# Kernel tuning notes

Hardware: AMD Instinct MI355X
Metric: run time of the kernel (lower is better)

Reference implementation:

```python
import jax, jax.numpy as jnp
import numpy as np

B, DIM, HID = 16384, 1024, 2048


def _ln(x, g, b, eps=1e-5):
    m = x.mean(-1, keepdims=True)
    v = ((x - m) ** 2).mean(-1, keepdims=True)
    return (x - m) / jnp.sqrt(v + eps) * g + b


def _attn1(x_kv, Wv, bv, Wo, bo):
    # seq-len-1 MHA: softmax over a single key is exactly 1 (per head),
    # so output = out_proj(v_proj(kv)); q/k projections cancel identically.
    return (x_kv @ Wv.T + bv) @ Wo.T + bo


def _ffn(x, W1, b1, W2, b2):
    return jnp.maximum(x @ W1.T + b1, 0.0) @ W2.T + b2


def setup_inputs() -> dict:
    key = jax.random.key(0)
    ks = iter(jax.random.split(key, 32))
    s = 0.02
    d = {
        'visual_feat': jax.random.normal(next(ks), (B, DIM), jnp.float32),
        'text_feat': jax.random.normal(next(ks), (B, DIM), jnp.float32),
    }
    for tag in ('sv', 'st', 'v2t', 't2v'):
        d[f'Wv_{tag}'] = jax.random.normal(next(ks), (DIM, DIM), jnp.float32) * s
        d[f'bv_{tag}'] = jnp.zeros((DIM,), jnp.float32)
        d[f'Wo_{tag}'] = jax.random.normal(next(ks), (DIM, DIM), jnp.float32) * s
        d[f'bo_{tag}'] = jnp.zeros((DIM,), jnp.float32)
    for tag in ('v1', 't1', 'v2', 't2'):
        d[f'g_{tag}'] = jnp.ones((DIM,), jnp.float32)
        d[f'be_{tag}'] = jnp.zeros((DIM,), jnp.float32)
    for tag in ('v', 't'):
        d[f'W1_{tag}'] = jax.random.normal(next(ks), (HID, DIM), jnp.float32) * s
        d[f'b1_{tag}'] = jnp.zeros((HID,), jnp.float32)
        d[f'W2_{tag}'] = jax.random.normal(next(ks), (DIM, HID), jnp.float32) * s
        d[f'b2_{tag}'] = jnp.zeros((DIM,), jnp.float32)
    return d


def reference(visual_feat, text_feat,
              Wv_sv, bv_sv, Wo_sv, bo_sv,
              Wv_st, bv_st, Wo_st, bo_st,
              Wv_v2t, bv_v2t, Wo_v2t, bo_v2t,
              Wv_t2v, bv_t2v, Wo_t2v, bo_t2v,
              g_v1, be_v1, g_t1, be_t1, g_v2, be_v2, g_t2, be_t2,
              W1_v, b1_v, W2_v, b2_v, W1_t, b1_t, W2_t, b2_t):
    v_self = _ln(visual_feat + _attn1(visual_feat, Wv_sv, bv_sv, Wo_sv, bo_sv), g_v1, be_v1)
    t_self = _ln(text_feat + _attn1(text_feat, Wv_st, bv_st, Wo_st, bo_st), g_t1, be_t1)
    v_cross = _attn1(t_self, Wv_v2t, bv_v2t, Wo_v2t, bo_v2t)  # v queries t -> depends on kv=t_self only
    t_cross = _attn1(v_self, Wv_t2v, bv_t2v, Wo_t2v, bo_t2v)
    v_fused = _ln(visual_feat + (v_self + v_cross) * 0.5, g_v2, be_v2)
    t_fused = _ln(text_feat + (t_self + t_cross) * 0.5, g_t2, be_t2)
    v_out = v_fused + _ffn(v_fused, W1_v, b1_v, W2_v, b2_v)
    t_out = t_fused + _ffn(t_fused, W1_t, b1_t, W2_t, b2_t)
    new_context = (v_out + t_out) * 0.5
    return (v_out, t_out, new_context)
```

## Files before the change

kernel.cpp:

```cpp
#include <hip/hip_runtime.h>
#include <stdint.h>


typedef unsigned short u16;
typedef __bf16 bf16x8 __attribute__((ext_vector_type(8)));
typedef float f32x4 __attribute__((ext_vector_type(4)));

__device__ __forceinline__ u16 f2bf(float f) {
    uint32_t x = __float_as_uint(f);
    uint32_t r = (x + 0x7fffu + ((x >> 16) & 1u)) >> 16;
    return (u16)r;
}
__device__ __forceinline__ float bf2f(u16 u) {
    return __uint_as_float(((uint32_t)u) << 16);
}

__device__ __forceinline__ void glds16(const u16* g, u16* l) {
    __builtin_amdgcn_global_load_lds(
        (__attribute__((address_space(1))) void*)g,
        (__attribute__((address_space(3))) void*)l, 16, 0, 0);
}

__global__ __launch_bounds__(256) void cvtk(const float* __restrict__ src,
                                            u16* __restrict__ dst) {
    size_t i = ((size_t)blockIdx.x * 256 + threadIdx.x) * 4;
    float4 v = *(const float4*)&src[i];
    ushort4 o;
    o.x = f2bf(v.x); o.y = f2bf(v.y); o.z = f2bf(v.z); o.w = f2bf(v.w);
    *(ushort4*)&dst[i] = o;
}

struct Ptr4 { const float* p[4]; };
__global__ __launch_bounds__(256) void tcvtk(Ptr4 src, u16* __restrict__ dst) {
    __shared__ float t[32][33];
    const int z = blockIdx.z;
    const float* s = src.p[z];
    const int bx = blockIdx.x * 32, by = blockIdx.y * 32;
    const int tx = threadIdx.x & 31, ty = threadIdx.x >> 5;
#pragma unroll
    for (int i = 0; i < 32; i += 8)
        t[ty + i][tx] = s[(size_t)(by + ty + i) * 1024 + bx + tx];
    __syncthreads();
    u16* d = dst + (size_t)z * (1024 * 1024);
#pragma unroll
    for (int i = 0; i < 32; i += 8)
        d[(size_t)(bx + ty + i) * 1024 + by + tx] = f2bf(t[tx][ty + i]);
}

struct BiasArgs { const float* Wo[4]; const float* bv[4]; const float* bo[4]; };
__global__ __launch_bounds__(256) void biask(BiasArgs a, float* __restrict__ out) {
    const int z = blockIdx.y;
    const int row = blockIdx.x * 4 + (threadIdx.x >> 6);
    const int lane = threadIdx.x & 63;
    const float* w = a.Wo[z] + (size_t)row * 1024 + lane * 16;
    const float* v = a.bv[z] + lane * 16;
    float s = 0.f;
#pragma unroll
    for (int i = 0; i < 16; i += 4) {
        float4 w4 = *(const float4*)&w[i];
        float4 v4 = *(const float4*)&v[i];
        s += w4.x * v4.x + w4.y * v4.y + w4.z * v4.z + w4.w * v4.w;
    }
#pragma unroll
    for (int o = 1; o < 64; o <<= 1) s += __shfl_xor(s, o);
    if (lane == 0) out[(size_t)z * 1024 + row] = s + a.bo[z][row];
}

__global__ __launch_bounds__(256) void ctxk(const float* __restrict__ a,
                                            const float* __restrict__ b,
                                            float* __restrict__ o) {
    size_t i = ((size_t)blockIdx.x * 256 + threadIdx.x) * 4;
    float4 va = *(const float4*)&a[i];
    float4 vb = *(const float4*)&b[i];
    float4 vo;
    vo.x = 0.5f * (va.x + vb.x); vo.y = 0.5f * (va.y + vb.y);
    vo.z = 0.5f * (va.z + vb.z); vo.w = 0.5f * (va.w + vb.w);
    *(float4*)&o[i] = vo;
}

__global__ __launch_bounds__(256) void ln_kernel(
    const float* __restrict__ x, const u16* __restrict__ a1,
    const u16* __restrict__ a2, float s,
    const float* __restrict__ g, const float* __restrict__ be,
    u16* __restrict__ out) {
    const int tid = threadIdx.x;
    const size_t base = (size_t)blockIdx.x * 1024;
    const int i0 = tid * 4;

    float4 xv = *(const float4*)&x[base + i0];
    ushort4 u1 = *(const ushort4*)&a1[base + i0];
    float add[4] = {bf2f(u1.x), bf2f(u1.y), bf2f(u1.z), bf2f(u1.w)};
    if (a2) {
        ushort4 u2 = *(const ushort4*)&a2[base + i0];
        add[0] += bf2f(u2.x); add[1] += bf2f(u2.y);
        add[2] += bf2f(u2.z); add[3] += bf2f(u2.w);
    }
    float v[4] = {xv.x, xv.y, xv.z, xv.w};
    float sum = 0.f, ss = 0.f;
#pragma unroll
    for (int j = 0; j < 4; ++j) {
        v[j] += s * add[j];
        sum += v[j];
        ss += v[j] * v[j];
    }
#pragma unroll
    for (int o = 1; o < 64; o <<= 1) {
        sum += __shfl_xor(sum, o);
        ss  += __shfl_xor(ss, o);
    }
    __shared__ float s1[4], s2[4];
    if ((tid & 63) == 0) { s1[tid >> 6] = sum; s2[tid >> 6] = ss; }
    __syncthreads();
    sum = s1[0] + s1[1] + s1[2] + s1[3];
    ss  = s2[0] + s2[1] + s2[2] + s2[3];
    const float mean = sum * (1.f / 1024.f);
    const float var  = ss * (1.f / 1024.f) - mean * mean;
    const float inv  = rsqrtf(var + 1e-5f);

    float4 gv = *(const float4*)&g[i0];
    float4 bv = *(const float4*)&be[i0];
    ushort4 o4;
    o4.x = f2bf((v[0] - mean) * inv * gv.x + bv.x);
    o4.y = f2bf((v[1] - mean) * inv * gv.y + bv.y);
    o4.z = f2bf((v[2] - mean) * inv * gv.z + bv.z);
    o4.w = f2bf((v[3] - mean) * inv * gv.w + bv.w);
    *(ushort4*)&out[base + i0] = o4;
}

#define GBAR()  asm volatile("s_barrier" ::: "memory")
#define LGKM0() asm volatile("s_waitcnt lgkmcnt(0)" ::: "memory")

#define PH_READ_A(mi0)                                                        \
    a0[0] = *(const bf16x8*)&LDS[b][0][0][arow + (mi0) * 512];                \
    a0[1] = *(const bf16x8*)&LDS[b][0][1][arow + (mi0) * 512];                \
    a1[0] = *(const bf16x8*)&LDS[b][0][0][arow + ((mi0) + 1) * 512];          \
    a1[1] = *(const bf16x8*)&LDS[b][0][1][arow + ((mi0) + 1) * 512];

#define PH_MFMA(mi0)                                                          \
    __builtin_amdgcn_s_setprio(1);                                            \
    _Pragma("unroll")                                                         \
    for (int ni = 0; ni < 4; ++ni) {                                          \
        acc[mi0][ni] = __builtin_amdgcn_mfma_f32_16x16x32_bf16(               \
            a0[0], bF[ni][0], acc[mi0][ni], 0, 0, 0);                         \
        acc[mi0][ni] = __builtin_amdgcn_mfma_f32_16x16x32_bf16(               \
            a0[1], bF[ni][1], acc[mi0][ni], 0, 0, 0);                         \
        acc[(mi0) + 1][ni] = __builtin_amdgcn_mfma_f32_16x16x32_bf16(         \
            a1[0], bF[ni][0], acc[(mi0) + 1][ni], 0, 0, 0);                   \
        acc[(mi0) + 1][ni] = __builtin_amdgcn_mfma_f32_16x16x32_bf16(         \
            a1[1], bF[ni][1], acc[(mi0) + 1][ni], 0, 0, 0);                   \
    }                                                                         \
    __builtin_amdgcn_s_setprio(0);

__global__ __launch_bounds__(512, 2) void gemm256(
    const u16* __restrict__ A, const u16* __restrict__ W,
    const float* __restrict__ bias,
    int M, int N, int K, int mode,
    const u16* __restrict__ resid,
    u16* __restrict__ out_bf, float* __restrict__ out_f,
    size_t sA, size_t sW, size_t sC) {
    __shared__ u16 LDS[2][2][2][8192];

    const int tid  = threadIdx.x;
    const int lane = tid & 63;
    const int wv   = tid >> 6;
    const int wm   = wv >> 2, wn = wv & 3;

    const int gx   = gridDim.x;
    const int nwg  = gx * gridDim.y;
    const int orig = blockIdx.y * gx + blockIdx.x;
    const int qq = nwg >> 3, rr = nwg & 7;
    const int xcd = orig & 7, loc = orig >> 3;
    const int wgid =
        (xcd < rr ? xcd * (qq + 1) : rr * (qq + 1) + (xcd - rr) * qq) + loc;
    const int M0 = (wgid / gx) * 256, N0 = (wgid % gx) * 256;

    const int z = blockIdx.z;
    A += (size_t)z * sA;
    W += (size_t)z * sW;

    const f32x4 fz = {0.f, 0.f, 0.f, 0.f};
    f32x4 acc[8][4];
#pragma unroll
    for (int i = 0; i < 8; ++i)
#pragma unroll
        for (int j = 0; j < 4; ++j) acc[i][j] = fz;

    const int rl = lane >> 2;
    const int gS = (lane & 3) ^ ((lane >> 3) & 3);
    const u16* aS = A + (size_t)(M0 + wv * 32 + rl) * K + gS * 8;
    const u16* bS = W + (size_t)(N0 + wv * 32 + rl) * K + gS * 8;
    const size_t cstep = (size_t)16 * K;

    const int lr = lane & 15, qf = lane >> 4;
    const int fsw  = ((qf ^ ((lr >> 1) & 3)) << 3);
    const int arow = (wm * 128 + lr) * 32 + fsw;
    const int brow = (wn * 64 + lr) * 32 + fsw;

    const int nt = K >> 6;

    auto STAGE = [&](int mat, int t, int kh) {
        const u16* src = (mat ? bS : aS) + t * 64 + kh * 32;
        u16* dst = &LDS[t & 1][mat][kh][wv * 1024];
        glds16(src, dst);
        glds16(src + cstep, dst + 512);
    };

    STAGE(0, 0, 0); STAGE(0, 0, 1);
    STAGE(1, 0, 0); STAGE(1, 0, 1);
    if (nt > 1) {
        STAGE(1, 1, 0); STAGE(1, 1, 1);
        asm volatile("s_waitcnt vmcnt(4)" ::: "memory");
    } else {
        asm volatile("s_waitcnt vmcnt(0)" ::: "memory");
    }
    GBAR();

    for (int t = 0; t < nt; ++t) {
        const int b = t & 1;
        bf16x8 bF[4][2], a0[2], a1[2];

        PH_READ_A(0);
#pragma unroll
        for (int ni = 0; ni < 4; ++ni) {
            bF[ni][0] = *(const bf16x8*)&LDS[b][1][0][brow + ni * 512];
            bF[ni][1] = *(const bf16x8*)&LDS[b][1][1][brow + ni * 512];
        }
        if (t + 1 < nt) STAGE(0, t + 1, 0);
        GBAR(); LGKM0();
        PH_MFMA(0);
        GBAR();

        PH_READ_A(2);
        if (t + 1 < nt) STAGE(0, t + 1, 1);
        GBAR(); LGKM0();
        PH_MFMA(2);
        GBAR();

        PH_READ_A(4);
        if (t + 2 < nt) STAGE(1, t + 2, 0);
        GBAR(); LGKM0();
        PH_MFMA(4);
        GBAR();

        PH_READ_A(6);
        if (t + 2 < nt) STAGE(1, t + 2, 1);
        GBAR(); LGKM0();
        PH_MFMA(6);
        if (t + 2 < nt) asm volatile("s_waitcnt vmcnt(4)" ::: "memory");
        else            asm volatile("s_waitcnt vmcnt(0)" ::: "memory");
        GBAR();
    }

    const int rb = M0 + wm * 128 + (qf << 2);
    const int cb = N0 + wn * 64 + lr;
    out_bf += (size_t)z * sC;
    out_f  += (size_t)z * sC;
#pragma unroll
    for (int mi = 0; mi < 8; ++mi) {
#pragma unroll
        for (int ni = 0; ni < 4; ++ni) {
            const int c = cb + ni * 16;
            const float bv = bias ? bias[c] : 0.f;
#pragma unroll
            for (int r = 0; r < 4; ++r) {
                const int rrw = rb + mi * 16 + r;
                float val = acc[mi][ni][r] + bv;
                if (mode == 0) {
                    out_bf[(size_t)rrw * N + c] = f2bf(val);
                } else if (mode == 1) {
                    out_bf[(size_t)rrw * N + c] = f2bf(val > 0.f ? val : 0.f);
                } else {
                    out_f[(size_t)rrw * N + c] =
                        val + bf2f(resid[(size_t)rrw * N + c]);
                }
            }
        }
    }
}

extern "C" void kernel_launch(void* const* d_in, const int* in_sizes, int n_in,
                              void* d_out, int out_size, void* d_ws, size_t ws_size,
                              hipStream_t stream) {
    const float* visual = (const float*)d_in[0];
    const float* text   = (const float*)d_in[1];
    const float* Wv_sv  = (const float*)d_in[2];
    const float* bv_sv  = (const float*)d_in[3];
    const float* Wo_sv  = (const float*)d_in[4];
    const float* bo_sv  = (const float*)d_in[5];
    const float* Wv_st  = (const float*)d_in[6];
    const float* bv_st  = (const float*)d_in[7];
    const float* Wo_st  = (const float*)d_in[8];
    const float* bo_st  = (const float*)d_in[9];
    const float* Wv_v2t = (const float*)d_in[10];
    const float* bv_v2t = (const float*)d_in[11];
    const float* Wo_v2t = (const float*)d_in[12];
    const float* bo_v2t = (const float*)d_in[13];
    const float* Wv_t2v = (const float*)d_in[14];
    const float* bv_t2v = (const float*)d_in[15];
    const float* Wo_t2v = (const float*)d_in[16];
    const float* bo_t2v = (const float*)d_in[17];
    const float* g_v1 = (const float*)d_in[18];
    const float* be_v1 = (const float*)d_in[19];
    const float* g_t1 = (const float*)d_in[20];
    const float* be_t1 = (const float*)d_in[21];
    const float* g_v2 = (const float*)d_in[22];
    const float* be_v2 = (const float*)d_in[23];
    const float* g_t2 = (const float*)d_in[24];
    const float* be_t2 = (const float*)d_in[25];
    const float* W1_v = (const float*)d_in[26];
    const float* b1_v = (const float*)d_in[27];
    const float* W2_v = (const float*)d_in[28];
    const float* b2_v = (const float*)d_in[29];
    const float* W1_t = (const float*)d_in[30];
    const float* b1_t = (const float*)d_in[31];
    const float* W2_t = (const float*)d_in[32];
    const float* b2_t = (const float*)d_in[33];

    const int Bsz = 16384, D = 1024, HID = 2048;
    const size_t SQ = (size_t)D * D;
    const size_t BD = (size_t)Bsz * D;

    u16* wb = (u16*)d_ws;
    u16* wWc   = wb + 0 * SQ;
    u16* wW1_v = wb + 4 * SQ;
    u16* wW2_v = wb + 6 * SQ;
    u16* wW1_t = wb + 8 * SQ;
    u16* wW2_t = wb + 10 * SQ;
    float* bcAll = (float*)(wb + 12 * SQ);
    u16* P0 = wb + 13 * SQ;
    u16* P1 = wb + 29 * SQ;
    u16* P2 = wb + 45 * SQ;
    u16* P3 = wb + 61 * SQ;
    u16* Hbuf = P0;
    u16* wWo  = P3;
    u16* wWvT = P3 + 4 * SQ;

    float* out0 = (float*)d_out;
    float* out1 = out0 + BD;
    float* out2 = out0 + 2 * BD;

    auto cvt = [&](const float* src, u16* dst, size_t n) {
        cvtk<<<dim3((unsigned)(n / 1024)), dim3(256), 0, stream>>>(src, dst);
    };
    auto gemm = [&](const u16* Am, const u16* Wm, const float* bias, int M,
                    int N, int K, int mode, const u16* resid, void* out,
                    int zdim, size_t sA, size_t sW, size_t sC) {
        dim3 grid((unsigned)(N / 256), (unsigned)(M / 256), (unsigned)zdim);
        gemm256<<<grid, dim3(512), 0, stream>>>(Am, Wm, bias, M, N, K, mode,
                                                resid, (u16*)out, (float*)out,
                                                sA, sW, sC);
    };
    auto ln = [&](const float* x, const u16* a1, const u16* a2, float s,
                  const float* g, const float* be, u16* out) {
        ln_kernel<<<dim3(Bsz), dim3(256), 0, stream>>>(x, a1, a2, s, g, be, out);
    };

    cvt(Wo_sv, wWo + 0 * SQ, SQ);
    cvt(Wo_st, wWo + 1 * SQ, SQ);
    cvt(Wo_v2t, wWo + 2 * SQ, SQ);
    cvt(Wo_t2v, wWo + 3 * SQ, SQ);
    Ptr4 wvp = {{Wv_sv, Wv_st, Wv_v2t, Wv_t2v}};
    tcvtk<<<dim3(32, 32, 4), dim3(256), 0, stream>>>(wvp, wWvT);
    cvt(W1_v, wW1_v, 2 * SQ); cvt(W2_v, wW2_v, 2 * SQ);
    cvt(W1_t, wW1_t, 2 * SQ); cvt(W2_t, wW2_t, 2 * SQ);

    gemm(wWo, wWvT, nullptr, D, D, D, 0, nullptr, wWc, 4, SQ, SQ, SQ);
    BiasArgs ba = {{Wo_sv, Wo_st, Wo_v2t, Wo_t2v},
                   {bv_sv, bv_st, bv_v2t, bv_t2v},
                   {bo_sv, bo_st, bo_v2t, bo_t2v}};
    biask<<<dim3(256, 4), dim3(256), 0, stream>>>(ba, bcAll);
    const float* bc_sv  = bcAll;
    const float* bc_st  = bcAll + 1024;
    const float* bc_v2t = bcAll + 2048;
    const float* bc_t2v = bcAll + 3072;

    cvt(visual, P0, BD);
    gemm(P0, wWc + 0 * SQ, bc_sv, Bsz, D, D, 0, nullptr, P1, 1, 0, 0, 0);
    ln(visual, P1, nullptr, 1.f, g_v1, be_v1, P1);
    cvt(text, P0, BD);
    gemm(P0, wWc + 1 * SQ, bc_st, Bsz, D, D, 0, nullptr, P2, 1, 0, 0, 0);
    ln(text, P2, nullptr, 1.f, g_t1, be_t1, P2);

    gemm(P2, wWc + 2 * SQ, bc_v2t, Bsz, D, D, 0, nullptr, P0, 1, 0, 0, 0);
    ln(visual, P1, P0, 0.5f, g_v2, be_v2, P3);
    gemm(P1, wWc + 3 * SQ, bc_t2v, Bsz, D, D, 0, nullptr, P0, 1, 0, 0, 0);
    ln(text, P2, P0, 0.5f, g_t2, be_t2, P2);

    gemm(P3, wW1_v, b1_v, Bsz, HID, D, 1, nullptr, Hbuf, 1, 0, 0, 0);
    gemm(Hbuf, wW2_v, b2_v, Bsz, D, HID, 2, P3, out0, 1, 0, 0, 0);
    gemm(P2, wW1_t, b1_t, Bsz, HID, D, 1, nullptr, Hbuf, 1, 0, 0, 0);
    gemm(Hbuf, wW2_t, b2_t, Bsz, D, HID, 2, P2, out1, 1, 0, 0, 0);

    ctxk<<<dim3((unsigned)(BD / 1024)), dim3(256), 0, stream>>>(out0, out1, out2);
}
```

Before: 1.122 ms.

## Batch visual/text branches into z-batched GEMM and LN launches, reorder MFMA phases

The visual and text branches are now processed together. Each GEMM pair and LayerNorm pair becomes a single launch with a z/y grid dimension, using per-z bias and residual strides, and the weight and bias conversions are merged into batched kernels. The GEMM inner loop now loads four A fragments and reuses the B fragments across two phases, replacing the previous two-row macro. This doubles the grid size per launch, which fills the GPU better and cuts launch count. In exchange the workspace footprint grows considerably and register usage in the main loop may change.

```diff
diff --git a/kernel.cpp b/kernel.cpp
--- a/kernel.cpp
+++ b/kernel.cpp
@@ -21,16 +21,17 @@
         (__attribute__((address_space(3))) void*)l, 16, 0, 0);
 }
 
-__global__ __launch_bounds__(256) void cvtk(const float* __restrict__ src,
-                                            u16* __restrict__ dst) {
+struct Ptr4 { const float* p[4]; };
+__global__ __launch_bounds__(256) void cvt4k(Ptr4 src, u16* __restrict__ dst,
+                                             size_t zstride) {
+    const int z = blockIdx.y;
     size_t i = ((size_t)blockIdx.x * 256 + threadIdx.x) * 4;
-    float4 v = *(const float4*)&src[i];
+    float4 v = *(const float4*)&src.p[z][i];
     ushort4 o;
     o.x = f2bf(v.x); o.y = f2bf(v.y); o.z = f2bf(v.z); o.w = f2bf(v.w);
-    *(ushort4*)&dst[i] = o;
-}
-
-struct Ptr4 { const float* p[4]; };
+    *(ushort4*)&dst[z * zstride + i] = o;
+}
+
 __global__ __launch_bounds__(256) void tcvtk(Ptr4 src, u16* __restrict__ dst) {
     __shared__ float t[32][33];
     const int z = blockIdx.z;
@@ -64,6 +65,18 @@
 #pragma unroll
     for (int o = 1; o < 64; o <<= 1) s += __shfl_xor(s, o);
     if (lane == 0) out[(size_t)z * 1024 + row] = s + a.bo[z][row];
+}
+
+__global__ __launch_bounds__(256) void copyb(const float* a, const float* b,
+                                             const float* c, const float* d,
+                                             float* __restrict__ o) {
+    int i = blockIdx.x * 1024 + threadIdx.x * 4;
+    float4 v;
+    if (i < 2048)      v = *(const float4*)&a[i];
+    else if (i < 4096) v = *(const float4*)&b[i - 2048];
+    else if (i < 5120) v = *(const float4*)&c[i - 4096];
+    else               v = *(const float4*)&d[i - 5120];
+    *(float4*)&o[i] = v;
 }
 
 __global__ __launch_bounds__(256) void ctxk(const float* __restrict__ a,
@@ -78,20 +91,21 @@
     *(float4*)&o[i] = vo;
 }
 
-__global__ __launch_bounds__(256) void ln_kernel(
-    const float* __restrict__ x, const u16* __restrict__ a1,
-    const u16* __restrict__ a2, float s,
-    const float* __restrict__ g, const float* __restrict__ be,
-    u16* __restrict__ out) {
+struct LnArgs {
+    const float* x[2]; const u16* a1[2]; const u16* a2[2];
+    const float* g[2]; const float* be[2]; u16* out[2]; float s;
+};
+__global__ __launch_bounds__(256) void ln2_kernel(LnArgs A) {
+    const int y = blockIdx.y;
     const int tid = threadIdx.x;
     const size_t base = (size_t)blockIdx.x * 1024;
     const int i0 = tid * 4;
 
-    float4 xv = *(const float4*)&x[base + i0];
-    ushort4 u1 = *(const ushort4*)&a1[base + i0];
+    float4 xv = *(const float4*)&A.x[y][base + i0];
+    ushort4 u1 = *(const ushort4*)&A.a1[y][base + i0];
     float add[4] = {bf2f(u1.x), bf2f(u1.y), bf2f(u1.z), bf2f(u1.w)};
-    if (a2) {
-        ushort4 u2 = *(const ushort4*)&a2[base + i0];
+    if (A.a2[y]) {
+        ushort4 u2 = *(const ushort4*)&A.a2[y][base + i0];
         add[0] += bf2f(u2.x); add[1] += bf2f(u2.y);
         add[2] += bf2f(u2.z); add[3] += bf2f(u2.w);
     }
@@ -99,7 +113,7 @@
     float sum = 0.f, ss = 0.f;
 #pragma unroll
     for (int j = 0; j < 4; ++j) {
-        v[j] += s * add[j];
+        v[j] += A.s * add[j];
         sum += v[j];
         ss += v[j] * v[j];
     }
@@ -117,39 +131,18 @@
     const float var  = ss * (1.f / 1024.f) - mean * mean;
     const float inv  = rsqrtf(var + 1e-5f);
 
-    float4 gv = *(const float4*)&g[i0];
-    float4 bv = *(const float4*)&be[i0];
+    float4 gv = *(const float4*)&A.g[y][i0];
+    float4 bv = *(const float4*)&A.be[y][i0];
     ushort4 o4;
     o4.x = f2bf((v[0] - mean) * inv * gv.x + bv.x);
     o4.y = f2bf((v[1] - mean) * inv * gv.y + bv.y);
     o4.z = f2bf((v[2] - mean) * inv * gv.z + bv.z);
     o4.w = f2bf((v[3] - mean) * inv * gv.w + bv.w);
-    *(ushort4*)&out[base + i0] = o4;
+    *(ushort4*)&A.out[y][base + i0] = o4;
 }
 
 #define GBAR()  asm volatile("s_barrier" ::: "memory")
 #define LGKM0() asm volatile("s_waitcnt lgkmcnt(0)" ::: "memory")
-
-#define PH_READ_A(mi0)                                                        \
-    a0[0] = *(const bf16x8*)&LDS[b][0][0][arow + (mi0) * 512];                \
-    a0[1] = *(const bf16x8*)&LDS[b][0][1][arow + (mi0) * 512];                \
-    a1[0] = *(const bf16x8*)&LDS[b][0][0][arow + ((mi0) + 1) * 512];          \
-    a1[1] = *(const bf16x8*)&LDS[b][0][1][arow + ((mi0) + 1) * 512];
-
-#define PH_MFMA(mi0)                                                          \
-    __builtin_amdgcn_s_setprio(1);                                            \
-    _Pragma("unroll")                                                         \
-    for (int ni = 0; ni < 4; ++ni) {                                          \
-        acc[mi0][ni] = __builtin_amdgcn_mfma_f32_16x16x32_bf16(               \
-            a0[0], bF[ni][0], acc[mi0][ni], 0, 0, 0);                         \
-        acc[mi0][ni] = __builtin_amdgcn_mfma_f32_16x16x32_bf16(               \
-            a0[1], bF[ni][1], acc[mi0][ni], 0, 0, 0);                         \
-        acc[(mi0) + 1][ni] = __builtin_amdgcn_mfma_f32_16x16x32_bf16(         \
-            a1[0], bF[ni][0], acc[(mi0) + 1][ni], 0, 0, 0);                   \
-        acc[(mi0) + 1][ni] = __builtin_amdgcn_mfma_f32_16x16x32_bf16(         \
-            a1[1], bF[ni][1], acc[(mi0) + 1][ni], 0, 0, 0);                   \
-    }                                                                         \
-    __builtin_amdgcn_s_setprio(0);
 
 __global__ __launch_bounds__(512, 2) void gemm256(
     const u16* __restrict__ A, const u16* __restrict__ W,
@@ -157,7 +150,7 @@
     int M, int N, int K, int mode,
     const u16* __restrict__ resid,
     u16* __restrict__ out_bf, float* __restrict__ out_f,
-    size_t sA, size_t sW, size_t sC) {
+    size_t sA, size_t sW, size_t sC, size_t sB, size_t sR) {
     __shared__ u16 LDS[2][2][2][8192];
 
     const int tid  = threadIdx.x;
@@ -217,35 +210,72 @@
 
     for (int t = 0; t < nt; ++t) {
         const int b = t & 1;
-        bf16x8 bF[4][2], a0[2], a1[2];
-
-        PH_READ_A(0);
-#pragma unroll
-        for (int ni = 0; ni < 4; ++ni) {
-            bF[ni][0] = *(const bf16x8*)&LDS[b][1][0][brow + ni * 512];
-            bF[ni][1] = *(const bf16x8*)&LDS[b][1][1][brow + ni * 512];
-        }
+        bf16x8 aF[4], bK[4];
+
+#pragma unroll
+        for (int mi = 0; mi < 4; ++mi)
+            aF[mi] = *(const bf16x8*)&LDS[b][0][0][arow + mi * 512];
+#pragma unroll
+        for (int ni = 0; ni < 4; ++ni)
+            bK[ni] = *(const bf16x8*)&LDS[b][1][0][brow + ni * 512];
         if (t + 1 < nt) STAGE(0, t + 1, 0);
         GBAR(); LGKM0();
-        PH_MFMA(0);
+        __builtin_amdgcn_s_setprio(1);
+#pragma unroll
+        for (int mi = 0; mi < 4; ++mi)
+#pragma unroll
+            for (int ni = 0; ni < 4; ++ni)
+                acc[mi][ni] = __builtin_amdgcn_mfma_f32_16x16x32_bf16(
+                    aF[mi], bK[ni], acc[mi][ni], 0, 0, 0);
+        __builtin_amdgcn_s_setprio(0);
         GBAR();
 
-        PH_READ_A(2);
+#pragma unroll
+        for (int mi = 0; mi < 4; ++mi)
+            aF[mi] = *(const bf16x8*)&LDS[b][0][0][arow + (mi + 4) * 512];
         if (t + 1 < nt) STAGE(0, t + 1, 1);
         GBAR(); LGKM0();
-        PH_MFMA(2);
+        __builtin_amdgcn_s_setprio(1);
+#pragma unroll
+        for (int mi = 0; mi < 4; ++mi)
+#pragma unroll
+            for (int ni = 0; ni < 4; ++ni)
+                acc[mi + 4][ni] = __builtin_amdgcn_mfma_f32_16x16x32_bf16(
+                    aF[mi], bK[ni], acc[mi + 4][ni], 0, 0, 0);
+        __builtin_amdgcn_s_setprio(0);
         GBAR();
 
-        PH_READ_A(4);
+#pragma unroll
+        for (int mi = 0; mi < 4; ++mi)
+            aF[mi] = *(const bf16x8*)&LDS[b][0][1][arow + mi * 512];
+#pragma unroll
+        for (int ni = 0; ni < 4; ++ni)
+            bK[ni] = *(const bf16x8*)&LDS[b][1][1][brow + ni * 512];
         if (t + 2 < nt) STAGE(1, t + 2, 0);
         GBAR(); LGKM0();
-        PH_MFMA(4);
+        __builtin_amdgcn_s_setprio(1);
+#pragma unroll
+        for (int mi = 0; mi < 4; ++mi)
+#pragma unroll
+            for (int ni = 0; ni < 4; ++ni)
+                acc[mi][ni] = __builtin_amdgcn_mfma_f32_16x16x32_bf16(
+                    aF[mi], bK[ni], acc[mi][ni], 0, 0, 0);
+        __builtin_amdgcn_s_setprio(0);
         GBAR();
 
-        PH_READ_A(6);
+#pragma unroll
+        for (int mi = 0; mi < 4; ++mi)
+            aF[mi] = *(const bf16x8*)&LDS[b][0][1][arow + (mi + 4) * 512];
         if (t + 2 < nt) STAGE(1, t + 2, 1);
         GBAR(); LGKM0();
-        PH_MFMA(6);
+        __builtin_amdgcn_s_setprio(1);
+#pragma unroll
+        for (int mi = 0; mi < 4; ++mi)
+#pragma unroll
+            for (int ni = 0; ni < 4; ++ni)
+                acc[mi + 4][ni] = __builtin_amdgcn_mfma_f32_16x16x32_bf16(
+                    aF[mi], bK[ni], acc[mi + 4][ni], 0, 0, 0);
+        __builtin_amdgcn_s_setprio(0);
         if (t + 2 < nt) asm volatile("s_waitcnt vmcnt(4)" ::: "memory");
         else            asm volatile("s_waitcnt vmcnt(0)" ::: "memory");
         GBAR();
@@ -255,12 +285,14 @@
     const int cb = N0 + wn * 64 + lr;
     out_bf += (size_t)z * sC;
     out_f  += (size_t)z * sC;
+    const float* bz = bias ? bias + (size_t)z * sB : nullptr;
+    const u16* rz = resid ? resid + (size_t)z * sR : nullptr;
 #pragma unroll
     for (int mi = 0; mi < 8; ++mi) {
 #pragma unroll
         for (int ni = 0; ni < 4; ++ni) {
             const int c = cb + ni * 16;
-            const float bv = bias ? bias[c] : 0.f;
+            const float bv = bz ? bz[c] : 0.f;
 #pragma unroll
             for (int r = 0; r < 4; ++r) {
                 const int rrw = rb + mi * 16 + r;
@@ -271,7 +303,7 @@
                     out_bf[(size_t)rrw * N + c] = f2bf(val > 0.f ? val : 0.f);
                 } else {
                     out_f[(size_t)rrw * N + c] =
-                        val + bf2f(resid[(size_t)rrw * N + c]);
+                        val + bf2f(rz[(size_t)rrw * N + c]);
                 }
             }
         }
@@ -321,75 +353,70 @@
     const size_t BD = (size_t)Bsz * D;
 
     u16* wb = (u16*)d_ws;
-    u16* wWc   = wb + 0 * SQ;
-    u16* wW1_v = wb + 4 * SQ;
-    u16* wW2_v = wb + 6 * SQ;
-    u16* wW1_t = wb + 8 * SQ;
-    u16* wW2_t = wb + 10 * SQ;
+    u16* wWc  = wb + 0 * SQ;
+    u16* wW1  = wb + 4 * SQ;
+    u16* wW2  = wb + 8 * SQ;
     float* bcAll = (float*)(wb + 12 * SQ);
-    u16* P0 = wb + 13 * SQ;
-    u16* P1 = wb + 29 * SQ;
-    u16* P2 = wb + 45 * SQ;
-    u16* P3 = wb + 61 * SQ;
-    u16* Hbuf = P0;
-    u16* wWo  = P3;
-    u16* wWvT = P3 + 4 * SQ;
+    float* bF1   = bcAll + 4096;
+    float* bF2   = bcAll + 8192;
+    u16* XA = wb + 16 * SQ;
+    u16* XS = wb + 48 * SQ;
+    u16* XC = wb + 80 * SQ;
+    u16* XF = wb + 112 * SQ;
+    u16* H  = wb + 144 * SQ;
+    u16* wWo  = wb + 208 * SQ;
+    u16* wWvT = wb + 212 * SQ;
 
     float* out0 = (float*)d_out;
     float* out1 = out0 + BD;
     float* out2 = out0 + 2 * BD;
 
-    auto cvt = [&](const float* src, u16* dst, size_t n) {
-        cvtk<<<dim3((unsigned)(n / 1024)), dim3(256), 0, stream>>>(src, dst);
-    };
     auto gemm = [&](const u16* Am, const u16* Wm, const float* bias, int M,
                     int N, int K, int mode, const u16* resid, void* out,
-                    int zdim, size_t sA, size_t sW, size_t sC) {
+                    int zdim, size_t sA, size_t sW, size_t sC, size_t sB,
+                    size_t sR) {
         dim3 grid((unsigned)(N / 256), (unsigned)(M / 256), (unsigned)zdim);
         gemm256<<<grid, dim3(512), 0, stream>>>(Am, Wm, bias, M, N, K, mode,
                                                 resid, (u16*)out, (float*)out,
-                                                sA, sW, sC);
+                                                sA, sW, sC, sB, sR);
     };
-    auto ln = [&](const float* x, const u16* a1, const u16* a2, float s,
-                  const float* g, const float* be, u16* out) {
-        ln_kernel<<<dim3(Bsz), dim3(256), 0, stream>>>(x, a1, a2, s, g, be, out);
-    };
-
-    cvt(Wo_sv, wWo + 0 * SQ, SQ);
-    cvt(Wo_st, wWo + 1 * SQ, SQ);
-    cvt(Wo_v2t, wWo + 2 * SQ, SQ);
-    cvt(Wo_t2v, wWo + 3 * SQ, SQ);
-    Ptr4 wvp = {{Wv_sv, Wv_st, Wv_v2t, Wv_t2v}};
+
+    Ptr4 wop = {{Wo_sv, Wo_st, Wo_t2v, Wo_v2t}};
+    cvt4k<<<dim3(1024, 4), dim3(256), 0, stream>>>(wop, wWo, SQ);
+    Ptr4 wvp = {{Wv_sv, Wv_st, Wv_t2v, Wv_v2t}};
     tcvtk<<<dim3(32, 32, 4), dim3(256), 0, stream>>>(wvp, wWvT);
-    cvt(W1_v, wW1_v, 2 * SQ); cvt(W2_v, wW2_v, 2 * SQ);
-    cvt(W1_t, wW1_t, 2 * SQ); cvt(W2_t, wW2_t, 2 * SQ);
-
-    gemm(wWo, wWvT, nullptr, D, D, D, 0, nullptr, wWc, 4, SQ, SQ, SQ);
-    BiasArgs ba = {{Wo_sv, Wo_st, Wo_v2t, Wo_t2v},
-                   {bv_sv, bv_st, bv_v2t, bv_t2v},
-                   {bo_sv, bo_st, bo_v2t, bo_t2v}};
+    Ptr4 w12 = {{W1_v, W1_t, W2_v, W2_t}};
+    cvt4k<<<dim3(2048, 4), dim3(256), 0, stream>>>(w12, wW1, 2 * SQ);
+    copyb<<<dim3(6), dim3(256), 0, stream>>>(b1_v, b1_t, b2_v, b2_t, bF1);
+
+    gemm(wWo, wWvT, nullptr, D, D, D, 0, nullptr, wWc, 4, SQ, SQ, SQ, 0, 0);
+    BiasArgs ba = {{Wo_sv, Wo_st, Wo_t2v, Wo_v2t},
+                   {bv_sv, bv_st, bv_t2v, bv_v2t},
+                   {bo_sv, bo_st, bo_t2v, bo_v2t}};
     biask<<<dim3(256, 4), dim3(256), 0, stream>>>(ba, bcAll);
-    const float* bc_sv  = bcAll;
-    const float* bc_st  = bcAll + 1024;
-    const float* bc_v2t = bcAll + 2048;
-    const float* bc_t2v = bcAll + 3072;
-
-    cvt(visual, P0, BD);
-    gemm(P0, wWc + 0 * SQ, bc_sv, Bsz, D, D, 0, nullptr, P1, 1, 0, 0, 0);
-    ln(visual, P1, nullptr, 1.f, g_v1, be_v1, P1);
-    cvt(text, P0, BD);
-    gemm(P0, wWc + 1 * SQ, bc_st, Bsz, D, D, 0, nullptr, P2, 1, 0, 0, 0);
-    ln(text, P2, nullptr, 1.f, g_t1, be_t1, P2);
-
-    gemm(P2, wWc + 2 * SQ, bc_v2t, Bsz, D, D, 0, nullptr, P0, 1, 0, 0, 0);
-    ln(visual, P1, P0, 0.5f, g_v2, be_v2, P3);
-    gemm(P1, wWc + 3 * SQ, bc_t2v, Bsz, D, D, 0, nullptr, P0, 1, 0, 0, 0);
-    ln(text, P2, P0, 0.5f, g_t2, be_t2, P2);
-
-    gemm(P3, wW1_v, b1_v, Bsz, HID, D, 1, nullptr, Hbuf, 1, 0, 0, 0);
-    gemm(Hbuf, wW2_v, b2_v, Bsz, D, HID, 2, P3, out0, 1, 0, 0, 0);
-    gemm(P2, wW1_t, b1_t, Bsz, HID, D, 1, nullptr, Hbuf, 1, 0, 0, 0);
-    gemm(Hbuf, wW2_t, b2_t, Bsz, D, HID, 2, P2, out1, 1, 0, 0, 0);
+
+    Ptr4 inp = {{visual, text, nullptr, nullptr}};
+    cvt4k<<<dim3(16384, 2), dim3(256), 0, stream>>>(inp, XA, BD);
+
+    gemm(XA, wWc, bcAll, Bsz, D, D, 0, nullptr, XS, 2, BD, SQ, BD, 1024, 0);
+    {
+        LnArgs la = {{visual, text}, {XS, XS + BD}, {nullptr, nullptr},
+                     {g_v1, g_t1}, {be_v1, be_t1}, {XS, XS + BD}, 1.f};
+        ln2_kernel<<<dim3(16384, 2), dim3(256), 0, stream>>>(la);
+    }
+
+    gemm(XS, wWc + 2 * SQ, bcAll + 2048, Bsz, D, D, 0, nullptr, XC, 2,
+         BD, SQ, BD, 1024, 0);
+    {
+        LnArgs la = {{visual, text}, {XS, XS + BD}, {XC + BD, XC},
+                     {g_v2, g_t2}, {be_v2, be_t2}, {XF, XF + BD}, 0.5f};
+        ln2_kernel<<<dim3(16384, 2), dim3(256), 0, stream>>>(la);
+    }
+
+    gemm(XF, wW1, bF1, Bsz, HID, D, 1, nullptr, H, 2, BD, 2 * SQ, 2 * BD,
+         2048, 0);
+    gemm(H, wW2, bF2, Bsz, D, HID, 2, XF, out0, 2, 2 * BD, 2 * SQ, BD,
+         1024, BD);
 
     ctxk<<<dim3((unsigned)(BD / 1024)), dim3(256), 0, stream>>>(out0, out1, out2);
 }
```

New measurement: 1.115 ms. Within noise of the previous version (-0.6%).
